# Kernel optimization log

Measured on AMD Instinct MI355X. Metric: run time of the kernel, lower is better.

## Reference

```python
import jax, jax.numpy as jnp
import numpy as np

NUM_HEADS = 6

def setup_inputs() -> dict:
    key = jax.random.key(0)
    ks = jax.random.split(key, 5)
    B, N, C = 4096, 49, 192
    nW = 64
    x = jax.random.normal(ks[0], (B, N, C), dtype=jnp.float32)
    mask = jax.random.normal(ks[1], (nW, 1, N, N), dtype=jnp.float32)
    w_qkv = jax.random.normal(ks[2], (C, 3 * C), dtype=jnp.float32) * (C ** -0.5)
    w_proj = jax.random.normal(ks[3], (C, C), dtype=jnp.float32) * (C ** -0.5)
    b_proj = jnp.zeros((C,), dtype=jnp.float32)
    return {"x": x, "mask": mask, "w_qkv": w_qkv, "w_proj": w_proj, "b_proj": b_proj}

def reference(x, mask, w_qkv, w_proj, b_proj):
    B, N, C = x.shape
    H = NUM_HEADS
    d = C // H
    nW = mask.shape[0]
    scale = d ** -0.5
    # fused QKV projection: [B, N, 3, H, d]
    qkv = (x @ w_qkv).reshape(B, N, 3, H, d)
    q = qkv[:, :, 0] * scale          # [B, N, H, d]
    k = qkv[:, :, 1]
    v = qkv[:, :, 2]
    # scaled attention scores per head: [B, H, N, N]
    attn = jnp.einsum('bnhd,bmhd->bhnm', q, k)
    # additive window mask, broadcast over heads
    attn = attn.reshape(B // nW, nW, H, N, N) + mask
    attn = attn.reshape(B, H, N, N)
    attn = jax.nn.softmax(attn, axis=-1)
    # attention-weighted values, back to [B, N, C]
    out = jnp.einsum('bhnm,bmhd->bnhd', attn, v).reshape(B, N, C)
    return out @ w_proj + b_proj
```

## Files before the change

kernel.cpp:

```cpp
#include <hip/hip_runtime.h>

using bf16_t = __bf16;
using bf16x4 = __bf16 __attribute__((ext_vector_type(4)));
using bf16x8 = __bf16 __attribute__((ext_vector_type(8)));
using f32x4  = float  __attribute__((ext_vector_type(4)));

#define MFMA16(a, b, c) __builtin_amdgcn_mfma_f32_16x16x32_bf16((a), (b), (c), 0, 0, 0)

__device__ __forceinline__ bf16x8 ld_b8_2x(const bf16_t* p) {
    bf16x4 lo = *(const bf16x4*)p;
    bf16x4 hi = *(const bf16x4*)(p + 4);
    bf16x8 r;
    r[0] = lo[0]; r[1] = lo[1]; r[2] = lo[2]; r[3] = lo[3];
    r[4] = hi[0]; r[5] = hi[1]; r[6] = hi[2]; r[7] = hi[3];
    return r;
}

__global__ void prep_weights(const float* __restrict__ wqkv,
                             const float* __restrict__ wproj,
                             bf16_t* __restrict__ wA,
                             bf16_t* __restrict__ w2B) {
    int idx = blockIdx.x * 256 + threadIdx.x;
    const int N1 = 36 * 6 * 64 * 8;
    if (idx < N1) {
        int j = idx & 7, L = (idx >> 3) & 63, q = idx >> 9;
        int ks = q % 6, mt = q / 6;
        int cc = ks * 32 + (L >> 4) * 8 + j;
        int ch = mt * 16 + (L & 15);
        wA[idx] = (bf16_t)wqkv[cc * 576 + ch];
    } else {
        int idx2 = idx - N1;
        if (idx2 < 6 * 12 * 64 * 8) {
            int j = idx2 & 7, L = (idx2 >> 3) & 63, q = idx2 >> 9;
            int nt = q % 12, ks = q / 12;
            int cc = ks * 32 + (L >> 4) * 8 + j;
            int ch = nt * 16 + (L & 15);
            w2B[idx2] = (bf16_t)wproj[cc * 192 + ch];
        }
    }
}

__global__ __launch_bounds__(1024, 4) void fused_window_attn(
    const float* __restrict__ x,
    const float* __restrict__ mask,
    const bf16_t* __restrict__ wA,
    const bf16_t* __restrict__ w2B,
    const float* __restrict__ bias,
    float* __restrict__ out)
{
    constexpr int QP  = 40;
    constexpr int VTP = 68;
    constexpr int PMP = 72;
    constexpr int AOP = 204;

    __shared__ __align__(16) char smem[145920];
    bf16_t* qS  = (bf16_t*)smem;
    bf16_t* kS  = qS + 15360;
    bf16_t* vT  = qS + 30720;
    bf16_t* pmS = qS + 43776;
    char*   pB  = smem + 96768;
    bf16_t* xS  = (bf16_t*)(smem + 96768);
    bf16_t* aoS = (bf16_t*)smem;

    const int b    = blockIdx.x;
    const int tid  = threadIdx.x;
    const int wid  = tid >> 6;
    const int lane = tid & 63;
    const int g    = lane >> 4;
    const int c    = lane & 15;

    const int mtc = wid & 3;
    const int g3  = wid >> 2;
    float bbv[3];
#pragma unroll
    for (int j = 0; j < 3; ++j) bbv[j] = bias[(g3 * 3 + j) * 16 + c];

    const float* xb = x + (size_t)b * (49 * 192);
    for (int ch4 = tid; ch4 < 64 * 48; ch4 += 1024) {
        int tok = ch4 / 48, c4 = ch4 % 48;
        f32x4 v = (f32x4){0.f, 0.f, 0.f, 0.f};
        if (tok < 49) v = *(const f32x4*)(xb + tok * 192 + c4 * 4);
        bf16x4 o = {(bf16_t)v[0], (bf16_t)v[1], (bf16_t)v[2], (bf16_t)v[3]};
        *(bf16x4*)(xS + tok * AOP + c4 * 4) = o;
    }
    const float* mw = mask + (size_t)(b & 63) * (49 * 49);
    for (int idx = tid; idx < 64 * 64; idx += 1024) {
        int i = idx >> 6, t = idx & 63;
        float v;
        if (t < 49) v = (i < 49) ? mw[i * 49 + t] : 0.0f;
        else        v = -1e30f;
        pmS[i * PMP + t] = (bf16_t)v;
    }
    __syncthreads();

    const int nmt = (wid < 4) ? 3 : 2;
    const int mt0 = (wid < 4) ? wid * 3 : 12 + (wid - 4) * 2;

    f32x4 acc[3][4];
#pragma unroll
    for (int m = 0; m < 3; ++m)
#pragma unroll
        for (int n = 0; n < 4; ++n) acc[m][n] = (f32x4){0.f, 0.f, 0.f, 0.f};

#pragma unroll
    for (int ks = 0; ks < 6; ++ks) {
        bf16x8 Bf[4];
#pragma unroll
        for (int nt = 0; nt < 4; ++nt)
            Bf[nt] = ld_b8_2x(xS + (nt * 16 + c) * AOP + ks * 32 + g * 8);
#pragma unroll
        for (int m = 0; m < 3; ++m) {
            if (m < nmt) {
                int mt = mt0 + m;
                bf16x8 Af = *(const bf16x8*)(wA + (((size_t)mt * 6 + ks) * 64 + lane) * 8);
#pragma unroll
                for (int nt = 0; nt < 4; ++nt)
                    acc[m][nt] = MFMA16(Af, Bf[nt], acc[m][nt]);
            }
        }
    }

#pragma unroll
    for (int m = 0; m < 3; ++m) {
        if (m < nmt) {
            int mt  = mt0 + m;
            int typ = mt / 12;
            int rel = (mt - typ * 12) * 16 + g * 4;
            int hh  = rel >> 5;
            int dd0 = rel & 31;
#pragma unroll
            for (int nt = 0; nt < 4; ++nt) {
                int tok = nt * 16 + c;
                f32x4 a = acc[m][nt];
                if (typ == 2) {
#pragma unroll
                    for (int r = 0; r < 4; ++r)
                        vT[hh * (32 * VTP) + (dd0 + r) * VTP + tok] = (bf16_t)a[r];
                } else {
                    bf16x4 v4 = {(bf16_t)a[0], (bf16_t)a[1], (bf16_t)a[2], (bf16_t)a[3]};
                    if (typ == 0) *(bf16x4*)(qS + hh * (64 * QP) + tok * QP + dd0) = v4;
                    else          *(bf16x4*)(kS + hh * (64 * QP) + tok * QP + dd0) = v4;
                }
            }
        }
    }
    __syncthreads();

    const int h = wid >> 1;
    const int u = wid & 1;

    bf16x8 Ak[4], Bq[2];
    if (wid < 12) {
        const bf16_t* qh = qS + h * (64 * QP);
        const bf16_t* kh = kS + h * (64 * QP);
#pragma unroll
        for (int mt = 0; mt < 4; ++mt)
            Ak[mt] = *(const bf16x8*)(kh + (mt * 16 + c) * QP + g * 8);
#pragma unroll
        for (int nl = 0; nl < 2; ++nl)
            Bq[nl] = *(const bf16x8*)(qh + ((2 * u + nl) * 16 + c) * QP + g * 8);
    }
    __syncthreads();

    if (wid < 12) {
        char*         Ph = pB + h * 8192;
        const bf16_t* vh = vT + h * (32 * VTP);

        f32x4 sacc[4][2];
#pragma unroll
        for (int mt = 0; mt < 4; ++mt)
#pragma unroll
            for (int nl = 0; nl < 2; ++nl) sacc[mt][nl] = (f32x4){0.f, 0.f, 0.f, 0.f};
#pragma unroll
        for (int mt = 0; mt < 4; ++mt)
#pragma unroll
            for (int nl = 0; nl < 2; ++nl)
                sacc[mt][nl] = MFMA16(Ak[mt], Bq[nl], sacc[mt][nl]);

        const float scale = 0.17677669529663687f;
#pragma unroll
        for (int nl = 0; nl < 2; ++nl) {
            int i = (2 * u + nl) * 16 + c;
            float s[16];
#pragma unroll
            for (int mt = 0; mt < 4; ++mt) {
                bf16x4 pmv = *(const bf16x4*)(pmS + i * PMP + mt * 16 + g * 4);
#pragma unroll
                for (int r = 0; r < 4; ++r)
                    s[mt * 4 + r] = sacc[mt][nl][r] * scale + (float)pmv[r];
            }
            float mx = fmaxf(
                fmaxf(fmaxf(fmaxf(s[0], s[1]), s[2]), fmaxf(fmaxf(s[3], s[4]), s[5])),
                fmaxf(fmaxf(fmaxf(s[6], s[7]), s[8]), fmaxf(fmaxf(s[9], s[10]), s[11])));
            mx = fmaxf(mx, fmaxf(fmaxf(s[12], s[13]), fmaxf(s[14], s[15])));
            mx = fmaxf(mx, __shfl_xor(mx, 16));
            mx = fmaxf(mx, __shfl_xor(mx, 32));
#pragma unroll
            for (int k2 = 0; k2 < 16; ++k2) s[k2] = __expf(s[k2] - mx);
            float s01 = (s[0] + s[1]) + (s[2] + s[3]);
            float s23 = (s[4] + s[5]) + (s[6] + s[7]);
            float s45 = (s[8] + s[9]) + (s[10] + s[11]);
            float s67 = (s[12] + s[13]) + (s[14] + s[15]);
            float sum = (s01 + s23) + (s45 + s67);
            sum += __shfl_xor(sum, 16);
            sum += __shfl_xor(sum, 32);
            float linv = 1.0f / sum;
#pragma unroll
            for (int mt = 0; mt < 4; ++mt) {
                int tc = 2 * mt + (g >> 1);
                bf16x4 p4 = {(bf16_t)(s[mt * 4 + 0] * linv), (bf16_t)(s[mt * 4 + 1] * linv),
                             (bf16_t)(s[mt * 4 + 2] * linv), (bf16_t)(s[mt * 4 + 3] * linv)};
                *(bf16x4*)(Ph + i * 128 + ((tc ^ (i & 7)) << 4) + ((g & 1) << 3)) = p4;
            }
        }

        f32x4 oacc[2][2];
#pragma unroll
        for (int a0 = 0; a0 < 2; ++a0)
#pragma unroll
            for (int a1 = 0; a1 < 2; ++a1) oacc[a0][a1] = (f32x4){0.f, 0.f, 0.f, 0.f};

#pragma unroll
        for (int ks = 0; ks < 2; ++ks) {
            bf16x8 Bv[2];
#pragma unroll
            for (int nd = 0; nd < 2; ++nd)
                Bv[nd] = ld_b8_2x(vh + (nd * 16 + c) * VTP + ks * 32 + g * 8);
#pragma unroll
            for (int nl = 0; nl < 2; ++nl) {
                int i = (2 * u + nl) * 16 + c;
                bf16x8 Ap = *(const bf16x8*)(Ph + i * 128 + (((4 * ks + g) ^ (i & 7)) << 4));
#pragma unroll
                for (int nd = 0; nd < 2; ++nd)
                    oacc[nl][nd] = MFMA16(Ap, Bv[nd], oacc[nl][nd]);
            }
        }

#pragma unroll
        for (int nl = 0; nl < 2; ++nl)
#pragma unroll
            for (int nd = 0; nd < 2; ++nd) {
                f32x4 o = oacc[nl][nd];
#pragma unroll
                for (int r = 0; r < 4; ++r) {
                    int i = (2 * u + nl) * 16 + 4 * g + r;
                    aoS[i * AOP + h * 32 + nd * 16 + c] = (bf16_t)o[r];
                }
            }
    }
    __syncthreads();

    f32x4 pacc[3];
#pragma unroll
    for (int j = 0; j < 3; ++j) pacc[j] = (f32x4){0.f, 0.f, 0.f, 0.f};

#pragma unroll
    for (int ks = 0; ks < 6; ++ks) {
        bf16x8 Ao = ld_b8_2x(aoS + (mtc * 16 + c) * AOP + ks * 32 + g * 8);
#pragma unroll
        for (int j = 0; j < 3; ++j) {
            bf16x8 Bw = *(const bf16x8*)(w2B + (((size_t)ks * 12 + g3 * 3 + j) * 64 + lane) * 8);
            pacc[j] = MFMA16(Ao, Bw, pacc[j]);
        }
    }

    float* ob = out + (size_t)b * (49 * 192);
#pragma unroll
    for (int j = 0; j < 3; ++j) {
        int ch2 = (g3 * 3 + j) * 16 + c;
        f32x4 a = pacc[j];
#pragma unroll
        for (int r = 0; r < 4; ++r) {
            int tok = mtc * 16 + 4 * g + r;
            if (tok < 49) ob[(size_t)tok * 192 + ch2] = a[r] + bbv[j];
        }
    }
}

extern "C" void kernel_launch(void* const* d_in, const int* in_sizes, int n_in,
                              void* d_out, int out_size, void* d_ws, size_t ws_size,
                              hipStream_t stream) {
    const float* x     = (const float*)d_in[0];
    const float* mask  = (const float*)d_in[1];
    const float* wqkv  = (const float*)d_in[2];
    const float* wproj = (const float*)d_in[3];
    const float* bias  = (const float*)d_in[4];
    float* out = (float*)d_out;

    bf16_t* wA  = (bf16_t*)d_ws;
    bf16_t* w2B = wA + 110592;

    prep_weights<<<576, 256, 0, stream>>>(wqkv, wproj, wA, w2B);
    fused_window_attn<<<4096, 1024, 0, stream>>>(x, mask, wA, w2B, bias, out);
}
```

Before: 408.7 us.

## Halve block size, shrink LDS, keep softmax probabilities in registers via shuffles

Moves the fused window-attention kernel from 1024 to 512 threads and cuts LDS from about 146 KB to about 81 KB by aliasing buffers, so more blocks can be resident per CU. The mask is read directly from global memory in the softmax instead of being staged in LDS. Softmax probabilities are packed into registers and redistributed into the MFMA operand layout with cross-lane shuffles, replacing the LDS round-trip through the P buffer. Each warp now does more of the QKV and output projection, and each attention warp handles a whole head. The cost is many more shuffles, uncoalesced scalar mask loads, and more serial work per warp.

```diff
diff --git a/kernel.cpp b/kernel.cpp
--- a/kernel.cpp
+++ b/kernel.cpp
@@ -40,7 +40,7 @@
     }
 }
 
-__global__ __launch_bounds__(1024, 4) void fused_window_attn(
+__global__ __launch_bounds__(512, 4) void fused_window_attn(
     const float* __restrict__ x,
     const float* __restrict__ mask,
     const bf16_t* __restrict__ wA,
@@ -48,19 +48,16 @@
     const float* __restrict__ bias,
     float* __restrict__ out)
 {
-    constexpr int QP  = 40;
+    constexpr int QP  = 36;
     constexpr int VTP = 68;
-    constexpr int PMP = 72;
     constexpr int AOP = 204;
 
-    __shared__ __align__(16) char smem[145920];
+    __shared__ __align__(16) char smem[81408];
     bf16_t* qS  = (bf16_t*)smem;
-    bf16_t* kS  = qS + 15360;
-    bf16_t* vT  = qS + 30720;
-    bf16_t* pmS = qS + 43776;
-    char*   pB  = smem + 96768;
-    bf16_t* xS  = (bf16_t*)(smem + 96768);
-    bf16_t* aoS = (bf16_t*)smem;
+    bf16_t* kS  = qS + 13824;
+    bf16_t* xS  = kS + 13824;
+    bf16_t* vT  = xS;
+    bf16_t* aoS = kS;
 
     const int b    = blockIdx.x;
     const int tid  = threadIdx.x;
@@ -70,204 +67,248 @@
     const int c    = lane & 15;
 
     const int mtc = wid & 3;
-    const int g3  = wid >> 2;
-    float bbv[3];
-#pragma unroll
-    for (int j = 0; j < 3; ++j) bbv[j] = bias[(g3 * 3 + j) * 16 + c];
+    const int g3  = wid >> 1 >> 1;
+    float bbv[6];
+#pragma unroll
+    for (int j = 0; j < 6; ++j) bbv[j] = bias[(g3 * 6 + j) * 16 + c];
 
     const float* xb = x + (size_t)b * (49 * 192);
-    for (int ch4 = tid; ch4 < 64 * 48; ch4 += 1024) {
+    for (int ch4 = tid; ch4 < 64 * 48; ch4 += 512) {
         int tok = ch4 / 48, c4 = ch4 % 48;
         f32x4 v = (f32x4){0.f, 0.f, 0.f, 0.f};
         if (tok < 49) v = *(const f32x4*)(xb + tok * 192 + c4 * 4);
         bf16x4 o = {(bf16_t)v[0], (bf16_t)v[1], (bf16_t)v[2], (bf16_t)v[3]};
         *(bf16x4*)(xS + tok * AOP + c4 * 4) = o;
     }
-    const float* mw = mask + (size_t)(b & 63) * (49 * 49);
-    for (int idx = tid; idx < 64 * 64; idx += 1024) {
-        int i = idx >> 6, t = idx & 63;
-        float v;
-        if (t < 49) v = (i < 49) ? mw[i * 49 + t] : 0.0f;
-        else        v = -1e30f;
-        pmS[i * PMP + t] = (bf16_t)v;
-    }
     __syncthreads();
 
-    const int nmt = (wid < 4) ? 3 : 2;
-    const int mt0 = (wid < 4) ? wid * 3 : 12 + (wid - 4) * 2;
-
-    f32x4 acc[3][4];
-#pragma unroll
-    for (int m = 0; m < 3; ++m)
-#pragma unroll
-        for (int n = 0; n < 4; ++n) acc[m][n] = (f32x4){0.f, 0.f, 0.f, 0.f};
-
-#pragma unroll
-    for (int ks = 0; ks < 6; ++ks) {
-        bf16x8 Bf[4];
+    const f32x4 ZV = (f32x4){0.f, 0.f, 0.f, 0.f};
+    f32x4 aA[4], aB[4], vacc0[4], vacc1[4];
+
+#define PASS2(MTA, MTB, ACCA, ACCB)                                            \
+    {                                                                          \
+        _Pragma("unroll") for (int n = 0; n < 4; ++n) {                        \
+            ACCA[n] = ZV; ACCB[n] = ZV;                                        \
+        }                                                                      \
+        _Pragma("unroll") for (int ks = 0; ks < 6; ++ks) {                     \
+            bf16x8 Bf[4];                                                      \
+            _Pragma("unroll") for (int nt = 0; nt < 4; ++nt)                   \
+                Bf[nt] = ld_b8_2x(xS + (nt * 16 + c) * AOP + ks * 32 + g * 8); \
+            bf16x8 AfA = *(const bf16x8*)(wA + (((size_t)(MTA) * 6 + ks) * 64 + lane) * 8); \
+            bf16x8 AfB = *(const bf16x8*)(wA + (((size_t)(MTB) * 6 + ks) * 64 + lane) * 8); \
+            _Pragma("unroll") for (int nt = 0; nt < 4; ++nt) {                 \
+                ACCA[nt] = MFMA16(AfA, Bf[nt], ACCA[nt]);                      \
+                ACCB[nt] = MFMA16(AfB, Bf[nt], ACCB[nt]);                      \
+            }                                                                  \
+        }                                                                      \
+    }
+
+    auto routeQK = [&](int mt, f32x4 (&acc)[4]) {
+        int typ = mt / 12;
+        int rel = (mt - typ * 12) * 16 + g * 4;
+        int hh  = rel >> 5;
+        int dd0 = rel & 31;
+        bf16_t* base = typ ? kS : qS;
+#pragma unroll
+        for (int nt = 0; nt < 4; ++nt) {
+            int tok = nt * 16 + c;
+            bf16x4 v4 = {(bf16_t)acc[nt][0], (bf16_t)acc[nt][1],
+                         (bf16_t)acc[nt][2], (bf16_t)acc[nt][3]};
+            *(bf16x4*)(base + hh * (64 * QP) + tok * QP + dd0) = v4;
+        }
+    };
+
+    PASS2(wid, wid + 8, aA, aB);
+    routeQK(wid, aA);
+    routeQK(wid + 8, aB);
+    PASS2(wid + 16, wid + 24, aA, vacc0);
+    routeQK(wid + 16, aA);
+    if (wid < 4) {
+#pragma unroll
+        for (int n = 0; n < 4; ++n) vacc1[n] = ZV;
+#pragma unroll
+        for (int ks = 0; ks < 6; ++ks) {
+            bf16x8 Bf[4];
+#pragma unroll
+            for (int nt = 0; nt < 4; ++nt)
+                Bf[nt] = ld_b8_2x(xS + (nt * 16 + c) * AOP + ks * 32 + g * 8);
+            bf16x8 Af = *(const bf16x8*)(wA + (((size_t)(wid + 32) * 6 + ks) * 64 + lane) * 8);
+#pragma unroll
+            for (int nt = 0; nt < 4; ++nt) vacc1[nt] = MFMA16(Af, Bf[nt], vacc1[nt]);
+        }
+    }
+    __syncthreads();
+
+    auto routeV = [&](int mt, f32x4 (&acc)[4]) {
+        int rel = (mt - 24) * 16 + g * 4;
+        int hh  = rel >> 5;
+        int dd0 = rel & 31;
 #pragma unroll
         for (int nt = 0; nt < 4; ++nt)
-            Bf[nt] = ld_b8_2x(xS + (nt * 16 + c) * AOP + ks * 32 + g * 8);
-#pragma unroll
-        for (int m = 0; m < 3; ++m) {
-            if (m < nmt) {
-                int mt = mt0 + m;
-                bf16x8 Af = *(const bf16x8*)(wA + (((size_t)mt * 6 + ks) * 64 + lane) * 8);
-#pragma unroll
-                for (int nt = 0; nt < 4; ++nt)
-                    acc[m][nt] = MFMA16(Af, Bf[nt], acc[m][nt]);
+#pragma unroll
+            for (int r = 0; r < 4; ++r)
+                vT[hh * (32 * VTP) + (dd0 + r) * VTP + nt * 16 + c] = (bf16_t)acc[nt][r];
+    };
+    routeV(wid + 24, vacc0);
+    if (wid < 4) routeV(wid + 32, vacc1);
+
+    const int h = wid;
+    bf16x8 Ak[4];
+    if (wid < 6) {
+        const bf16_t* kh = kS + h * (64 * QP);
+#pragma unroll
+        for (int mt = 0; mt < 4; ++mt)
+            Ak[mt] = ld_b8_2x(kh + (mt * 16 + c) * QP + g * 8);
+    }
+    __syncthreads();
+
+    if (wid < 6) {
+        const bf16_t* qh = qS + h * (64 * QP);
+        const bf16_t* vh = vT + h * (32 * VTP);
+        const float*  mw = mask + (size_t)(b & 63) * (49 * 49);
+        const float   scale = 0.17677669529663687f;
+        const int  L1s = ((lane >> 4) & 1) * 32 + c;
+        const int  L2s = L1s + 16;
+        const bool hisel = (g >= 2);
+
+#pragma unroll
+        for (int u = 0; u < 2; ++u) {
+            bf16x8 Bq[2];
+#pragma unroll
+            for (int nl = 0; nl < 2; ++nl)
+                Bq[nl] = ld_b8_2x(qh + ((u * 2 + nl) * 16 + c) * QP + g * 8);
+            f32x4 sacc[4][2];
+#pragma unroll
+            for (int mt = 0; mt < 4; ++mt)
+#pragma unroll
+                for (int nl = 0; nl < 2; ++nl) sacc[mt][nl] = ZV;
+#pragma unroll
+            for (int mt = 0; mt < 4; ++mt)
+#pragma unroll
+                for (int nl = 0; nl < 2; ++nl)
+                    sacc[mt][nl] = MFMA16(Ak[mt], Bq[nl], sacc[mt][nl]);
+
+            unsigned int D[2][4][2];
+#pragma unroll
+            for (int nl = 0; nl < 2; ++nl) {
+                int i = u * 32 + nl * 16 + c;
+                float s[16];
+#pragma unroll
+                for (int mt = 0; mt < 4; ++mt) {
+                    int t0 = mt * 16 + g * 4;
+                    float pmv[4];
+                    if (i < 49) {
+                        if (mt < 3) {
+                            const float* mp = mw + i * 49 + t0;
+                            pmv[0] = mp[0]; pmv[1] = mp[1];
+                            pmv[2] = mp[2]; pmv[3] = mp[3];
+                        } else {
+#pragma unroll
+                            for (int r = 0; r < 4; ++r)
+                                pmv[r] = (t0 + r < 49) ? mw[i * 49 + t0 + r] : -1e30f;
+                        }
+                    } else {
+#pragma unroll
+                        for (int r = 0; r < 4; ++r)
+                            pmv[r] = (t0 + r < 49) ? 0.0f : -1e30f;
+                    }
+#pragma unroll
+                    for (int r = 0; r < 4; ++r)
+                        s[mt * 4 + r] = sacc[mt][nl][r] * scale + pmv[r];
+                }
+                float m0 = fmaxf(fmaxf(fmaxf(s[0], s[1]), fmaxf(s[2], s[3])),
+                                 fmaxf(fmaxf(s[4], s[5]), fmaxf(s[6], s[7])));
+                float m1 = fmaxf(fmaxf(fmaxf(s[8], s[9]), fmaxf(s[10], s[11])),
+                                 fmaxf(fmaxf(s[12], s[13]), fmaxf(s[14], s[15])));
+                float mx = fmaxf(m0, m1);
+                mx = fmaxf(mx, __shfl_xor(mx, 16));
+                mx = fmaxf(mx, __shfl_xor(mx, 32));
+#pragma unroll
+                for (int k2 = 0; k2 < 16; ++k2) s[k2] = __expf(s[k2] - mx);
+                float s01 = (s[0] + s[1]) + (s[2] + s[3]);
+                float s23 = (s[4] + s[5]) + (s[6] + s[7]);
+                float s45 = (s[8] + s[9]) + (s[10] + s[11]);
+                float s67 = (s[12] + s[13]) + (s[14] + s[15]);
+                float sum = (s01 + s23) + (s45 + s67);
+                sum += __shfl_xor(sum, 16);
+                sum += __shfl_xor(sum, 32);
+                float linv = 1.0f / sum;
+#pragma unroll
+                for (int mt = 0; mt < 4; ++mt)
+#pragma unroll
+                    for (int h2 = 0; h2 < 2; ++h2) {
+                        union { __bf16 hh2[2]; unsigned int uu; } bp;
+                        bp.hh2[0] = (bf16_t)(s[mt * 4 + 2 * h2] * linv);
+                        bp.hh2[1] = (bf16_t)(s[mt * 4 + 2 * h2 + 1] * linv);
+                        D[nl][mt][h2] = bp.uu;
+                    }
             }
-        }
-    }
-
-#pragma unroll
-    for (int m = 0; m < 3; ++m) {
-        if (m < nmt) {
-            int mt  = mt0 + m;
-            int typ = mt / 12;
-            int rel = (mt - typ * 12) * 16 + g * 4;
-            int hh  = rel >> 5;
-            int dd0 = rel & 31;
-#pragma unroll
-            for (int nt = 0; nt < 4; ++nt) {
-                int tok = nt * 16 + c;
-                f32x4 a = acc[m][nt];
-                if (typ == 2) {
-#pragma unroll
-                    for (int r = 0; r < 4; ++r)
-                        vT[hh * (32 * VTP) + (dd0 + r) * VTP + tok] = (bf16_t)a[r];
-                } else {
-                    bf16x4 v4 = {(bf16_t)a[0], (bf16_t)a[1], (bf16_t)a[2], (bf16_t)a[3]};
-                    if (typ == 0) *(bf16x4*)(qS + hh * (64 * QP) + tok * QP + dd0) = v4;
-                    else          *(bf16x4*)(kS + hh * (64 * QP) + tok * QP + dd0) = v4;
+
+            f32x4 oacc[2][2];
+#pragma unroll
+            for (int a0 = 0; a0 < 2; ++a0)
+#pragma unroll
+                for (int a1 = 0; a1 < 2; ++a1) oacc[a0][a1] = ZV;
+#pragma unroll
+            for (int ks = 0; ks < 2; ++ks) {
+                bf16x8 Bv[2];
+#pragma unroll
+                for (int nd = 0; nd < 2; ++nd)
+                    Bv[nd] = ld_b8_2x(vh + (nd * 16 + c) * VTP + ks * 32 + g * 8);
+#pragma unroll
+                for (int nl = 0; nl < 2; ++nl) {
+                    unsigned int a0 = (unsigned)__shfl((int)D[nl][2 * ks][0], L1s);
+                    unsigned int b0 = (unsigned)__shfl((int)D[nl][2 * ks + 1][0], L1s);
+                    unsigned int a1 = (unsigned)__shfl((int)D[nl][2 * ks][1], L1s);
+                    unsigned int b1 = (unsigned)__shfl((int)D[nl][2 * ks + 1][1], L1s);
+                    unsigned int a2 = (unsigned)__shfl((int)D[nl][2 * ks][0], L2s);
+                    unsigned int b2 = (unsigned)__shfl((int)D[nl][2 * ks + 1][0], L2s);
+                    unsigned int a3 = (unsigned)__shfl((int)D[nl][2 * ks][1], L2s);
+                    unsigned int b3 = (unsigned)__shfl((int)D[nl][2 * ks + 1][1], L2s);
+                    union { unsigned int uu[4]; bf16x8 v; } ap;
+                    ap.uu[0] = hisel ? b0 : a0;
+                    ap.uu[1] = hisel ? b1 : a1;
+                    ap.uu[2] = hisel ? b2 : a2;
+                    ap.uu[3] = hisel ? b3 : a3;
+#pragma unroll
+                    for (int nd = 0; nd < 2; ++nd)
+                        oacc[nl][nd] = MFMA16(ap.v, Bv[nd], oacc[nl][nd]);
                 }
             }
+
+#pragma unroll
+            for (int nl = 0; nl < 2; ++nl)
+#pragma unroll
+                for (int nd = 0; nd < 2; ++nd) {
+                    f32x4 o = oacc[nl][nd];
+#pragma unroll
+                    for (int r = 0; r < 4; ++r) {
+                        int i = u * 32 + nl * 16 + 4 * g + r;
+                        aoS[i * AOP + h * 32 + nd * 16 + c] = (bf16_t)o[r];
+                    }
+                }
         }
     }
     __syncthreads();
 
-    const int h = wid >> 1;
-    const int u = wid & 1;
-
-    bf16x8 Ak[4], Bq[2];
-    if (wid < 12) {
-        const bf16_t* qh = qS + h * (64 * QP);
-        const bf16_t* kh = kS + h * (64 * QP);
-#pragma unroll
-        for (int mt = 0; mt < 4; ++mt)
-            Ak[mt] = *(const bf16x8*)(kh + (mt * 16 + c) * QP + g * 8);
-#pragma unroll
-        for (int nl = 0; nl < 2; ++nl)
-            Bq[nl] = *(const bf16x8*)(qh + ((2 * u + nl) * 16 + c) * QP + g * 8);
-    }
-    __syncthreads();
-
-    if (wid < 12) {
-        char*         Ph = pB + h * 8192;
-        const bf16_t* vh = vT + h * (32 * VTP);
-
-        f32x4 sacc[4][2];
-#pragma unroll
-        for (int mt = 0; mt < 4; ++mt)
-#pragma unroll
-            for (int nl = 0; nl < 2; ++nl) sacc[mt][nl] = (f32x4){0.f, 0.f, 0.f, 0.f};
-#pragma unroll
-        for (int mt = 0; mt < 4; ++mt)
-#pragma unroll
-            for (int nl = 0; nl < 2; ++nl)
-                sacc[mt][nl] = MFMA16(Ak[mt], Bq[nl], sacc[mt][nl]);
-
-        const float scale = 0.17677669529663687f;
-#pragma unroll
-        for (int nl = 0; nl < 2; ++nl) {
-            int i = (2 * u + nl) * 16 + c;
-            float s[16];
-#pragma unroll
-            for (int mt = 0; mt < 4; ++mt) {
-                bf16x4 pmv = *(const bf16x4*)(pmS + i * PMP + mt * 16 + g * 4);
-#pragma unroll
-                for (int r = 0; r < 4; ++r)
-                    s[mt * 4 + r] = sacc[mt][nl][r] * scale + (float)pmv[r];
-            }
-            float mx = fmaxf(
-                fmaxf(fmaxf(fmaxf(s[0], s[1]), s[2]), fmaxf(fmaxf(s[3], s[4]), s[5])),
-                fmaxf(fmaxf(fmaxf(s[6], s[7]), s[8]), fmaxf(fmaxf(s[9], s[10]), s[11])));
-            mx = fmaxf(mx, fmaxf(fmaxf(s[12], s[13]), fmaxf(s[14], s[15])));
-            mx = fmaxf(mx, __shfl_xor(mx, 16));
-            mx = fmaxf(mx, __shfl_xor(mx, 32));
-#pragma unroll
-            for (int k2 = 0; k2 < 16; ++k2) s[k2] = __expf(s[k2] - mx);
-            float s01 = (s[0] + s[1]) + (s[2] + s[3]);
-            float s23 = (s[4] + s[5]) + (s[6] + s[7]);
-            float s45 = (s[8] + s[9]) + (s[10] + s[11]);
-            float s67 = (s[12] + s[13]) + (s[14] + s[15]);
-            float sum = (s01 + s23) + (s45 + s67);
-            sum += __shfl_xor(sum, 16);
-            sum += __shfl_xor(sum, 32);
-            float linv = 1.0f / sum;
-#pragma unroll
-            for (int mt = 0; mt < 4; ++mt) {
-                int tc = 2 * mt + (g >> 1);
-                bf16x4 p4 = {(bf16_t)(s[mt * 4 + 0] * linv), (bf16_t)(s[mt * 4 + 1] * linv),
-                             (bf16_t)(s[mt * 4 + 2] * linv), (bf16_t)(s[mt * 4 + 3] * linv)};
-                *(bf16x4*)(Ph + i * 128 + ((tc ^ (i & 7)) << 4) + ((g & 1) << 3)) = p4;
-            }
-        }
-
-        f32x4 oacc[2][2];
-#pragma unroll
-        for (int a0 = 0; a0 < 2; ++a0)
-#pragma unroll
-            for (int a1 = 0; a1 < 2; ++a1) oacc[a0][a1] = (f32x4){0.f, 0.f, 0.f, 0.f};
-
-#pragma unroll
-        for (int ks = 0; ks < 2; ++ks) {
-            bf16x8 Bv[2];
-#pragma unroll
-            for (int nd = 0; nd < 2; ++nd)
-                Bv[nd] = ld_b8_2x(vh + (nd * 16 + c) * VTP + ks * 32 + g * 8);
-#pragma unroll
-            for (int nl = 0; nl < 2; ++nl) {
-                int i = (2 * u + nl) * 16 + c;
-                bf16x8 Ap = *(const bf16x8*)(Ph + i * 128 + (((4 * ks + g) ^ (i & 7)) << 4));
-#pragma unroll
-                for (int nd = 0; nd < 2; ++nd)
-                    oacc[nl][nd] = MFMA16(Ap, Bv[nd], oacc[nl][nd]);
-            }
-        }
-
-#pragma unroll
-        for (int nl = 0; nl < 2; ++nl)
-#pragma unroll
-            for (int nd = 0; nd < 2; ++nd) {
-                f32x4 o = oacc[nl][nd];
-#pragma unroll
-                for (int r = 0; r < 4; ++r) {
-                    int i = (2 * u + nl) * 16 + 4 * g + r;
-                    aoS[i * AOP + h * 32 + nd * 16 + c] = (bf16_t)o[r];
-                }
-            }
-    }
-    __syncthreads();
-
-    f32x4 pacc[3];
-#pragma unroll
-    for (int j = 0; j < 3; ++j) pacc[j] = (f32x4){0.f, 0.f, 0.f, 0.f};
+    f32x4 pacc[6];
+#pragma unroll
+    for (int j = 0; j < 6; ++j) pacc[j] = ZV;
 
 #pragma unroll
     for (int ks = 0; ks < 6; ++ks) {
         bf16x8 Ao = ld_b8_2x(aoS + (mtc * 16 + c) * AOP + ks * 32 + g * 8);
 #pragma unroll
-        for (int j = 0; j < 3; ++j) {
-            bf16x8 Bw = *(const bf16x8*)(w2B + (((size_t)ks * 12 + g3 * 3 + j) * 64 + lane) * 8);
+        for (int j = 0; j < 6; ++j) {
+            bf16x8 Bw = *(const bf16x8*)(w2B + (((size_t)ks * 12 + g3 * 6 + j) * 64 + lane) * 8);
             pacc[j] = MFMA16(Ao, Bw, pacc[j]);
         }
     }
 
     float* ob = out + (size_t)b * (49 * 192);
 #pragma unroll
-    for (int j = 0; j < 3; ++j) {
-        int ch2 = (g3 * 3 + j) * 16 + c;
+    for (int j = 0; j < 6; ++j) {
+        int ch2 = (g3 * 6 + j) * 16 + c;
         f32x4 a = pacc[j];
 #pragma unroll
         for (int r = 0; r < 4; ++r) {
@@ -275,6 +316,7 @@
             if (tok < 49) ob[(size_t)tok * 192 + ch2] = a[r] + bbv[j];
         }
     }
+#undef PASS2
 }
 
 extern "C" void kernel_launch(void* const* d_in, const int* in_sizes, int n_in,
@@ -291,5 +333,5 @@
     bf16_t* w2B = wA + 110592;
 
     prep_weights<<<576, 256, 0, stream>>>(wqkv, wproj, wA, w2B);
-    fused_window_attn<<<4096, 1024, 0, stream>>>(x, mask, wA, w2B, bias, out);
+    fused_window_attn<<<4096, 512, 0, stream>>>(x, mask, wA, w2B, bias, out);
 }
```

Result: faster. 376.2 us (-7.9%).
